# Performance work log

Measured on AMD Instinct MI355X. Metric: run time of the kernel, lower is better.

## Reference

```python
import jax, jax.numpy as jnp
import numpy as np
from jax import lax

B, CIN, H, W = 32, 128, 64, 64
COUT, K, NK, HID = 128, 3, 4, 32
TEMP = 34.0
PAD = 1


def setup_inputs() -> dict:
    key = jax.random.key(0)
    k1, k2, k3, k4 = jax.random.split(key, 4)
    x = jax.random.normal(k1, (B, CIN, H, W), dtype=jnp.float32)
    fc1_w = jax.random.normal(k2, (HID, CIN), dtype=jnp.float32) * (2.0 / CIN) ** 0.5
    fc2_w = jax.random.normal(k3, (NK, HID), dtype=jnp.float32) * (2.0 / HID) ** 0.5
    fc2_b = jnp.zeros((NK,), dtype=jnp.float32)
    weight = jax.random.normal(k4, (NK, COUT, CIN, K, K), dtype=jnp.float32) * 0.05
    bias = jnp.zeros((NK, COUT), dtype=jnp.float32)
    return {"x": x, "fc1_w": fc1_w, "fc2_w": fc2_w, "fc2_b": fc2_b,
            "weight": weight, "bias": bias}


def _per_sample_conv(xi, wi):
    # xi: [CIN, H, W], wi: [COUT, CIN, K, K]
    out = lax.conv_general_dilated(
        xi[None], wi,
        window_strides=(1, 1),
        padding=[(PAD, PAD), (PAD, PAD)],
        dimension_numbers=("NCHW", "OIHW", "NCHW"))
    return out[0]  # [COUT, H', W']


def reference(x, fc1_w, fc2_w, fc2_b, weight, bias):
    # attention: global avg pool -> 1x1 conv (matmul) -> relu -> 1x1 conv -> softmax
    context = jnp.mean(x, axis=(2, 3))                      # [B, CIN]
    hid = jax.nn.relu(context @ fc1_w.T)                    # [B, HID]
    logits = hid @ fc2_w.T + fc2_b                          # [B, NK]
    att = jax.nn.softmax(logits / TEMP, axis=1)             # [B, NK]
    # aggregate per-sample kernels and biases
    agg_w = jnp.einsum("bk,koihw->boihw", att, weight)      # [B, COUT, CIN, K, K]
    agg_b = att @ bias                                      # [B, COUT]
    # per-sample convolution (equivalent to the groups=B trick in torch)
    out = jax.vmap(_per_sample_conv)(x, agg_w)              # [B, COUT, H, W]
    return out + agg_b[:, :, None, None]
```

## Files before the change

### kernel.cpp

```cpp
#include <hip/hip_runtime.h>

#define B_    32
#define CIN_  128
#define H_    64
#define W_    64
#define COUT_ 128
#define NK_   4
#define HID_  32
#define TEMP_ 34.0f

typedef short bf16x8 __attribute__((ext_vector_type(8)));
typedef float f32x16 __attribute__((ext_vector_type(16)));

__device__ __forceinline__ short f2bf(float f) {
    union { float f; unsigned u; } c; c.f = f;
    unsigned r = (c.u + 0x7FFFu + ((c.u >> 16) & 1u)) >> 16;
    return (short)r;
}

__global__ __launch_bounds__(64) void k_context(const float* __restrict__ x,
                                                float* __restrict__ ctx) {
    const int bc = blockIdx.x;
    const float* p = x + (size_t)bc * (H_ * W_);
    const int lane = threadIdx.x;
    float s = 0.f;
    for (int i = lane * 4; i < H_ * W_; i += 64 * 4) {
        float4 v = *(const float4*)(p + i);
        s += v.x + v.y + v.z + v.w;
    }
    for (int off = 32; off > 0; off >>= 1) s += __shfl_down(s, off, 64);
    if (lane == 0) ctx[bc] = s * (1.0f / (H_ * W_));
}

__global__ __launch_bounds__(256) void k_aggw(const float* __restrict__ ctx,
        const float* __restrict__ fc1w, const float* __restrict__ fc2w,
        const float* __restrict__ fc2b, const float* __restrict__ bias,
        const float* __restrict__ weight, short* __restrict__ aggwt,
        float* __restrict__ aggb) {
    __shared__ float hidp[8][32];
    __shared__ float shid[32];
    __shared__ float satt[NK_];
    __shared__ float sbuf[2304];
    const int t = threadIdx.x;
    const int blk = blockIdx.x;
    const int b = blk >> 6;
    const int co0 = (blk & 63) * 2;
    {
        const int hh = t & 31, part = t >> 5;
        const float* c  = ctx + b * CIN_ + part * 16;
        const float* f1 = fc1w + hh * CIN_ + part * 16;
        float s = 0.f;
#pragma unroll
        for (int j = 0; j < 16; ++j) s += c[j] * f1[j];
        hidp[part][hh] = s;
    }
    __syncthreads();
    if (t < 32) {
        float s = 0.f;
#pragma unroll
        for (int p = 0; p < 8; ++p) s += hidp[p][t];
        shid[t] = fmaxf(s, 0.f);
    }
    __syncthreads();
    if (t == 0) {
        float lg[NK_]; float mx = -1e30f;
#pragma unroll
        for (int k = 0; k < NK_; ++k) {
            float s = fc2b[k];
            for (int hh = 0; hh < HID_; ++hh) s += shid[hh] * fc2w[k * HID_ + hh];
            lg[k] = s / TEMP_; mx = fmaxf(mx, lg[k]);
        }
        float den = 0.f;
#pragma unroll
        for (int k = 0; k < NK_; ++k) { lg[k] = expf(lg[k] - mx); den += lg[k]; }
        const float rd = 1.0f / den;
#pragma unroll
        for (int k = 0; k < NK_; ++k) satt[k] = lg[k] * rd;
    }
    __syncthreads();
    const float a0 = satt[0], a1 = satt[1], a2 = satt[2], a3 = satt[3];

    if ((t & 127) == 0) {
        const int co = co0 + (t >> 7);
        aggb[b * COUT_ + co] = a0 * bias[co] + a1 * bias[COUT_ + co]
                             + a2 * bias[2 * COUT_ + co] + a3 * bias[3 * COUT_ + co];
    }

    const size_t kstride = (size_t)COUT_ * CIN_ * 9;
    const float* W0 = weight + (size_t)co0 * (CIN_ * 9);
#pragma unroll
    for (int jj = 0; jj < 3; ++jj) {
        const int i4 = jj * 256 + t;
        if (i4 < 576) {
            const float4 w0 = *(const float4*)(W0 + i4 * 4);
            const float4 w1 = *(const float4*)(W0 + kstride + i4 * 4);
            const float4 w2 = *(const float4*)(W0 + 2 * kstride + i4 * 4);
            const float4 w3 = *(const float4*)(W0 + 3 * kstride + i4 * 4);
            float4 r;
            r.x = a0 * w0.x + a1 * w1.x + a2 * w2.x + a3 * w3.x;
            r.y = a0 * w0.y + a1 * w1.y + a2 * w2.y + a3 * w3.y;
            r.z = a0 * w0.z + a1 * w1.z + a2 * w2.z + a3 * w3.z;
            r.w = a0 * w0.w + a1 * w1.w + a2 * w2.w + a3 * w3.w;
            *(float4*)(&sbuf[i4 * 4]) = r;
        }
    }
    __syncthreads();
#pragma unroll
    for (int jj = 0; jj < 2; ++jj) {
        const int g = jj * 256 + t;
        if (g < 288) {
            const int coL = (g >= 144) ? 1 : 0;
            const int gg = g - coL * 144;
            const int r  = gg >> 4;
            const int oc = gg & 15;
            const int co = co0 + coL;
            bf16x8 v;
#pragma unroll
            for (int e = 0; e < 8; ++e)
                v[e] = f2bf(sbuf[(coL * 128 + oc * 8 + e) * 9 + r]);
            short* dst = aggwt
                + ((size_t)(((b * 4 + (co >> 5)) * 9 + r) * 8 + (oc >> 1)) * 512)
                + ((co & 31) * 2 + (oc & 1)) * 8;
            *(bf16x8*)dst = v;
        }
    }
}

#define RBY 8448
#define RSH 4224
__global__ __launch_bounds__(256, 2) void k_conv(const float* __restrict__ x,
        const short* __restrict__ aggwt, const float* __restrict__ aggb,
        float* __restrict__ out) {
    __shared__ short xt[6 * RSH];
    const int tid = threadIdx.x;
    const int blk = blockIdx.x;
    const int b = blk & 31;
    const int h0 = (blk >> 5) * 4;
    const int lane = tid & 63;
    const int wv = tid >> 6;
    const int l31 = lane & 31;
    const int lane5 = lane >> 5;

    if (tid < 96) {
        const int row = tid >> 4;
        const int q = tid & 15;
        const int cl = (q < 8) ? q : (512 + q);
        *(int4*)(&xt[row * RSH + cl * 8]) = make_int4(0, 0, 0, 0);
    }

    f32x16 acc[8];
#pragma unroll
    for (int t = 0; t < 8; ++t)
#pragma unroll
        for (int k = 0; k < 16; ++k) acc[t][k] = 0.f;

    const short* Ap = aggwt + (size_t)(b * 4 + wv) * (9 * 8 * 512)
                            + (size_t)(l31 * 2 + lane5) * 8;

#pragma unroll
    for (int k = 0; k < 12; ++k) {
        const int task = k * 4 + wv;
        const int row = task >> 3;
        const int g = task & 7;
        const int in_h = h0 - 1 + row;
        bf16x8 v = (bf16x8){0, 0, 0, 0, 0, 0, 0, 0};
        if (in_h >= 0 && in_h < H_) {
            const float* gp = x + (((size_t)b * CIN_ + g * 8) * H_ + in_h) * W_ + lane;
            float f[8];
#pragma unroll
            for (int j = 0; j < 8; ++j) f[j] = gp[j * (H_ * W_)];
#pragma unroll
            for (int j = 0; j < 8; ++j) v[j] = f2bf(f[j]);
        }
        *(bf16x8*)(&xt[row * RSH + ((lane + 1) * 8 + ((g + lane) & 7)) * 8]) = v;
    }
    __syncthreads();

#pragma unroll
    for (int kc = 0; kc < 8; ++kc) {
        float sf[3][8];
        if (kc < 4) {
#pragma unroll
            for (int k = 0; k < 3; ++k) {
                const int task = k * 4 + wv;
                const int row = task >> 1;
                const int j = task & 1;
                const int in_h = h0 - 1 + row;
                if (in_h >= 0 && in_h < H_) {
                    const float* gp = x + (((size_t)b * CIN_ + 64 + (2 * kc + j) * 8) * H_
                                           + in_h) * W_ + lane;
#pragma unroll
                    for (int jj = 0; jj < 8; ++jj) sf[k][jj] = gp[jj * (H_ * W_)];
                }
            }
        }
        bf16x8 av[9];
#pragma unroll
        for (int r = 0; r < 9; ++r)
            av[r] = *(const bf16x8*)(Ap + ((size_t)(r * 8 + kc)) * 512);
        const int kcl = kc & 3;
        __builtin_amdgcn_s_setprio(1);
#pragma unroll
        for (int ir = 0; ir < 6; ++ir) {
            bf16x8 bv[2][3];
#pragma unroll
            for (int i = 0; i < 2; ++i)
#pragma unroll
                for (int kw = 0; kw < 3; ++kw) {
                    const int s = i * 32 + l31 + kw;
                    const int off = 16 * ((2 * kcl + lane5 + s - 1) & 7);
                    bv[i][kw] = *(const bf16x8*)((const char*)xt + ir * RBY + s * 128 + off);
                }
#pragma unroll
            for (int orr = 0; orr < 4; ++orr) {
                if (orr <= ir && ir <= orr + 2) {
                    const int kh = ir - orr;
#pragma unroll
                    for (int i = 0; i < 2; ++i)
#pragma unroll
                        for (int kw = 0; kw < 3; ++kw)
                            acc[orr * 2 + i] = __builtin_amdgcn_mfma_f32_32x32x16_bf16(
                                av[kh * 3 + kw], bv[i][kw], acc[orr * 2 + i], 0, 0, 0);
                }
            }
        }
        __builtin_amdgcn_s_setprio(0);
        if (kc <= 4) __syncthreads();
        if (kc < 4) {
#pragma unroll
            for (int k = 0; k < 3; ++k) {
                const int task = k * 4 + wv;
                const int row = task >> 1;
                const int j = task & 1;
                const int in_h = h0 - 1 + row;
                const int g = 2 * kc + j;
                bf16x8 v = (bf16x8){0, 0, 0, 0, 0, 0, 0, 0};
                if (in_h >= 0 && in_h < H_) {
#pragma unroll
                    for (int jj = 0; jj < 8; ++jj) v[jj] = f2bf(sf[k][jj]);
                }
                *(bf16x8*)(&xt[row * RSH + ((lane + 1) * 8 + ((g + lane) & 7)) * 8]) = v;
            }
        }
    }

    const float* ab = aggb + b * COUT_;
#pragma unroll
    for (int orr = 0; orr < 4; ++orr) {
#pragma unroll
        for (int i = 0; i < 2; ++i) {
            const int hh = h0 + orr;
            const int w = i * 32 + l31;
            float* op = out + ((size_t)b * COUT_ * H_ + hh) * W_ + w;
            const f32x16 a = acc[orr * 2 + i];
#pragma unroll
            for (int reg = 0; reg < 16; ++reg) {
                const int co = wv * 32 + (reg & 3) + 8 * (reg >> 2) + 4 * lane5;
                op[(size_t)co * (H_ * W_)] = a[reg] + ab[co];
            }
        }
    }
}

extern "C" void kernel_launch(void* const* d_in, const int* in_sizes, int n_in,
                              void* d_out, int out_size, void* d_ws, size_t ws_size,
                              hipStream_t stream) {
    const float* x    = (const float*)d_in[0];
    const float* fc1w = (const float*)d_in[1];
    const float* fc2w = (const float*)d_in[2];
    const float* fc2b = (const float*)d_in[3];
    const float* wgt  = (const float*)d_in[4];
    const float* bias = (const float*)d_in[5];
    float* out = (float*)d_out;

    char* ws = (char*)d_ws;
    float* ctx   = (float*)(ws + 0);
    float* aggb  = (float*)(ws + 16384);
    short* aggwt = (short*)(ws + 65536);

    k_context<<<dim3(B_ * CIN_), dim3(64), 0, stream>>>(x, ctx);
    k_aggw<<<dim3(B_ * (COUT_ / 2)), dim3(256), 0, stream>>>(
        ctx, fc1w, fc2w, fc2b, bias, wgt, aggwt, aggb);
    k_conv<<<dim3(B_ * (H_ / 4)), dim3(256), 0, stream>>>(x, aggwt, aggb, out);
}
```

Before: 165.4 us.

## Fuse context, weight aggregation and conv into one cooperative kernel with grid syncs

Replaces the three separate launches (pooling, attention/weight aggregation, conv) with one cooperative kernel of 512 blocks. Two grid-wide barriers separate the phases, and each phase's work is remapped onto the 512 blocks. The shared-memory tile is unioned with the aggregation scratch. The goal is to remove launch gaps and tail effects between the small pre-conv kernels. In exchange it depends on all 512 blocks being co-resident (2 per CU), pays the cost of the grid syncs, and falls back to the old path if the cooperative launch fails.

```diff
diff --git a/kernel.cpp b/kernel.cpp
--- a/kernel.cpp
+++ b/kernel.cpp
@@ -1,4 +1,6 @@
 #include <hip/hip_runtime.h>
+#include <hip/hip_cooperative_groups.h>
+namespace cg = cooperative_groups;
 
 #define B_    32
 #define CIN_  128
@@ -16,6 +18,255 @@
     union { float f; unsigned u; } c; c.f = f;
     unsigned r = (c.u + 0x7FFFu + ((c.u >> 16) & 1u)) >> 16;
     return (short)r;
+}
+
+#define RBY 8448
+#define RSH 4224
+
+__global__ __launch_bounds__(256, 2) void k_fused(
+        const float* __restrict__ x, const float* __restrict__ fc1w,
+        const float* __restrict__ fc2w, const float* __restrict__ fc2b,
+        const float* __restrict__ weight, const float* __restrict__ bias,
+        float* __restrict__ out, float* __restrict__ ctx,
+        short* __restrict__ aggwt, float* __restrict__ aggb) {
+    __shared__ union {
+        short xt[6 * RSH];
+        struct {
+            float hidp[8][32];
+            float shid[32];
+            float satt[NK_];
+            float sbuf[9216];
+        } p2;
+    } sm;
+    const int tid = threadIdx.x;
+    const int blk = blockIdx.x;
+
+    {
+        const int row = blk * 8 + (tid >> 5);
+        const int l32 = tid & 31;
+        const float* p = x + (size_t)row * (H_ * W_);
+        float s = 0.f;
+#pragma unroll
+        for (int k = 0; k < 32; ++k) {
+            float4 v = *(const float4*)(p + l32 * 4 + k * 128);
+            s += v.x + v.y + v.z + v.w;
+        }
+#pragma unroll
+        for (int off = 16; off > 0; off >>= 1) s += __shfl_down(s, off, 32);
+        if (l32 == 0) ctx[row] = s * (1.0f / (H_ * W_));
+    }
+    cg::this_grid().sync();
+
+    {
+        const int b2 = blk >> 4;
+        const int co0 = (blk & 15) * 8;
+        {
+            const int hh = tid & 31, part = tid >> 5;
+            const float* c  = ctx + b2 * CIN_ + part * 16;
+            const float* f1 = fc1w + hh * CIN_ + part * 16;
+            float s = 0.f;
+#pragma unroll
+            for (int j = 0; j < 16; ++j) s += c[j] * f1[j];
+            sm.p2.hidp[part][hh] = s;
+        }
+        __syncthreads();
+        if (tid < 32) {
+            float s = 0.f;
+#pragma unroll
+            for (int p = 0; p < 8; ++p) s += sm.p2.hidp[p][tid];
+            sm.p2.shid[tid] = fmaxf(s, 0.f);
+        }
+        __syncthreads();
+        if (tid == 0) {
+            float lg[NK_]; float mx = -1e30f;
+#pragma unroll
+            for (int k = 0; k < NK_; ++k) {
+                float s = fc2b[k];
+                for (int hh = 0; hh < HID_; ++hh) s += sm.p2.shid[hh] * fc2w[k * HID_ + hh];
+                lg[k] = s / TEMP_; mx = fmaxf(mx, lg[k]);
+            }
+            float den = 0.f;
+#pragma unroll
+            for (int k = 0; k < NK_; ++k) { lg[k] = expf(lg[k] - mx); den += lg[k]; }
+            const float rd = 1.0f / den;
+#pragma unroll
+            for (int k = 0; k < NK_; ++k) sm.p2.satt[k] = lg[k] * rd;
+        }
+        __syncthreads();
+        const float a0 = sm.p2.satt[0], a1 = sm.p2.satt[1],
+                    a2 = sm.p2.satt[2], a3 = sm.p2.satt[3];
+
+        if (tid < 8) {
+            const int co = co0 + tid;
+            aggb[b2 * COUT_ + co] = a0 * bias[co] + a1 * bias[COUT_ + co]
+                                  + a2 * bias[2 * COUT_ + co] + a3 * bias[3 * COUT_ + co];
+        }
+
+        const size_t kstride = (size_t)COUT_ * CIN_ * 9;
+        const float* W0 = weight + (size_t)co0 * (CIN_ * 9);
+#pragma unroll
+        for (int jj = 0; jj < 9; ++jj) {
+            const int i4 = jj * 256 + tid;
+            const float4 w0 = *(const float4*)(W0 + i4 * 4);
+            const float4 w1 = *(const float4*)(W0 + kstride + i4 * 4);
+            const float4 w2 = *(const float4*)(W0 + 2 * kstride + i4 * 4);
+            const float4 w3 = *(const float4*)(W0 + 3 * kstride + i4 * 4);
+            float4 r;
+            r.x = a0 * w0.x + a1 * w1.x + a2 * w2.x + a3 * w3.x;
+            r.y = a0 * w0.y + a1 * w1.y + a2 * w2.y + a3 * w3.y;
+            r.z = a0 * w0.z + a1 * w1.z + a2 * w2.z + a3 * w3.z;
+            r.w = a0 * w0.w + a1 * w1.w + a2 * w2.w + a3 * w3.w;
+            *(float4*)(&sm.p2.sbuf[i4 * 4]) = r;
+        }
+        __syncthreads();
+#pragma unroll
+        for (int jj = 0; jj < 5; ++jj) {
+            const int g = jj * 256 + tid;
+            if (g < 1152) {
+                const int coL = g / 144;
+                const int gg = g - coL * 144;
+                const int r  = gg >> 4;
+                const int oc = gg & 15;
+                const int co = co0 + coL;
+                bf16x8 v;
+#pragma unroll
+                for (int e = 0; e < 8; ++e)
+                    v[e] = f2bf(sm.p2.sbuf[(coL * 128 + oc * 8 + e) * 9 + r]);
+                short* dst = aggwt
+                    + ((size_t)(((b2 * 4 + (co >> 5)) * 9 + r) * 8 + (oc >> 1)) * 512)
+                    + ((co & 31) * 2 + (oc & 1)) * 8;
+                *(bf16x8*)dst = v;
+            }
+        }
+    }
+    cg::this_grid().sync();
+
+    const int b = blk & 31;
+    const int h0 = (blk >> 5) * 4;
+    const int lane = tid & 63;
+    const int wv = tid >> 6;
+    const int l31 = lane & 31;
+    const int lane5 = lane >> 5;
+
+    if (tid < 96) {
+        const int row = tid >> 4;
+        const int q = tid & 15;
+        const int cl = (q < 8) ? q : (512 + q);
+        *(int4*)(&sm.xt[row * RSH + cl * 8]) = make_int4(0, 0, 0, 0);
+    }
+
+    f32x16 acc[8];
+#pragma unroll
+    for (int t = 0; t < 8; ++t)
+#pragma unroll
+        for (int k = 0; k < 16; ++k) acc[t][k] = 0.f;
+
+    const short* Ap = aggwt + (size_t)(b * 4 + wv) * (9 * 8 * 512)
+                            + (size_t)(l31 * 2 + lane5) * 8;
+
+#pragma unroll
+    for (int k = 0; k < 12; ++k) {
+        const int task = k * 4 + wv;
+        const int row = task >> 3;
+        const int g = task & 7;
+        const int in_h = h0 - 1 + row;
+        bf16x8 v = (bf16x8){0, 0, 0, 0, 0, 0, 0, 0};
+        if (in_h >= 0 && in_h < H_) {
+            const float* gp = x + (((size_t)b * CIN_ + g * 8) * H_ + in_h) * W_ + lane;
+            float f[8];
+#pragma unroll
+            for (int j = 0; j < 8; ++j) f[j] = gp[j * (H_ * W_)];
+#pragma unroll
+            for (int j = 0; j < 8; ++j) v[j] = f2bf(f[j]);
+        }
+        *(bf16x8*)(&sm.xt[row * RSH + ((lane + 1) * 8 + ((g + lane) & 7)) * 8]) = v;
+    }
+    __syncthreads();
+
+#pragma unroll
+    for (int kc = 0; kc < 8; ++kc) {
+        float sf[3][8];
+        if (kc < 4) {
+#pragma unroll
+            for (int k = 0; k < 3; ++k) {
+                const int task = k * 4 + wv;
+                const int row = task >> 1;
+                const int j = task & 1;
+                const int in_h = h0 - 1 + row;
+                if (in_h >= 0 && in_h < H_) {
+                    const float* gp = x + (((size_t)b * CIN_ + 64 + (2 * kc + j) * 8) * H_
+                                           + in_h) * W_ + lane;
+#pragma unroll
+                    for (int jj = 0; jj < 8; ++jj) sf[k][jj] = gp[jj * (H_ * W_)];
+                }
+            }
+        }
+        bf16x8 av[9];
+#pragma unroll
+        for (int r = 0; r < 9; ++r)
+            av[r] = *(const bf16x8*)(Ap + ((size_t)(r * 8 + kc)) * 512);
+        const int kcl = kc & 3;
+        __builtin_amdgcn_s_setprio(1);
+#pragma unroll
+        for (int ir = 0; ir < 6; ++ir) {
+            bf16x8 bv[2][3];
+#pragma unroll
+            for (int i = 0; i < 2; ++i)
+#pragma unroll
+                for (int kw = 0; kw < 3; ++kw) {
+                    const int s = i * 32 + l31 + kw;
+                    const int off = 16 * ((2 * kcl + lane5 + s - 1) & 7);
+                    bv[i][kw] = *(const bf16x8*)((const char*)sm.xt + ir * RBY + s * 128 + off);
+                }
+#pragma unroll
+            for (int orr = 0; orr < 4; ++orr) {
+                if (orr <= ir && ir <= orr + 2) {
+                    const int kh = ir - orr;
+#pragma unroll
+                    for (int i = 0; i < 2; ++i)
+#pragma unroll
+                        for (int kw = 0; kw < 3; ++kw)
+                            acc[orr * 2 + i] = __builtin_amdgcn_mfma_f32_32x32x16_bf16(
+                                av[kh * 3 + kw], bv[i][kw], acc[orr * 2 + i], 0, 0, 0);
+                }
+            }
+        }
+        __builtin_amdgcn_s_setprio(0);
+        if (kc <= 4) __syncthreads();
+        if (kc < 4) {
+#pragma unroll
+            for (int k = 0; k < 3; ++k) {
+                const int task = k * 4 + wv;
+                const int row = task >> 1;
+                const int j = task & 1;
+                const int in_h = h0 - 1 + row;
+                const int g = 2 * kc + j;
+                bf16x8 v = (bf16x8){0, 0, 0, 0, 0, 0, 0, 0};
+                if (in_h >= 0 && in_h < H_) {
+#pragma unroll
+                    for (int jj = 0; jj < 8; ++jj) v[jj] = f2bf(sf[k][jj]);
+                }
+                *(bf16x8*)(&sm.xt[row * RSH + ((lane + 1) * 8 + ((g + lane) & 7)) * 8]) = v;
+            }
+        }
+    }
+
+    const float* ab = aggb + b * COUT_;
+#pragma unroll
+    for (int orr = 0; orr < 4; ++orr) {
+#pragma unroll
+        for (int i = 0; i < 2; ++i) {
+            const int hh = h0 + orr;
+            const int w = i * 32 + l31;
+            float* op = out + ((size_t)b * COUT_ * H_ + hh) * W_ + w;
+            const f32x16 a = acc[orr * 2 + i];
+#pragma unroll
+            for (int reg = 0; reg < 16; ++reg) {
+                const int co = wv * 32 + (reg & 3) + 8 * (reg >> 2) + 4 * lane5;
+                op[(size_t)co * (H_ * W_)] = a[reg] + ab[co];
+            }
+        }
+    }
 }
 
 __global__ __launch_bounds__(64) void k_context(const float* __restrict__ x,
@@ -79,13 +330,11 @@
     }
     __syncthreads();
     const float a0 = satt[0], a1 = satt[1], a2 = satt[2], a3 = satt[3];
-
     if ((t & 127) == 0) {
         const int co = co0 + (t >> 7);
         aggb[b * COUT_ + co] = a0 * bias[co] + a1 * bias[COUT_ + co]
                              + a2 * bias[2 * COUT_ + co] + a3 * bias[3 * COUT_ + co];
     }
-
     const size_t kstride = (size_t)COUT_ * CIN_ * 9;
     const float* W0 = weight + (size_t)co0 * (CIN_ * 9);
 #pragma unroll
@@ -126,8 +375,6 @@
     }
 }
 
-#define RBY 8448
-#define RSH 4224
 __global__ __launch_bounds__(256, 2) void k_conv(const float* __restrict__ x,
         const short* __restrict__ aggwt, const float* __restrict__ aggb,
         float* __restrict__ out) {
@@ -140,23 +387,19 @@
     const int wv = tid >> 6;
     const int l31 = lane & 31;
     const int lane5 = lane >> 5;
-
     if (tid < 96) {
         const int row = tid >> 4;
         const int q = tid & 15;
         const int cl = (q < 8) ? q : (512 + q);
         *(int4*)(&xt[row * RSH + cl * 8]) = make_int4(0, 0, 0, 0);
     }
-
     f32x16 acc[8];
 #pragma unroll
     for (int t = 0; t < 8; ++t)
 #pragma unroll
         for (int k = 0; k < 16; ++k) acc[t][k] = 0.f;
-
     const short* Ap = aggwt + (size_t)(b * 4 + wv) * (9 * 8 * 512)
                             + (size_t)(l31 * 2 + lane5) * 8;
-
 #pragma unroll
     for (int k = 0; k < 12; ++k) {
         const int task = k * 4 + wv;
@@ -175,7 +418,6 @@
         *(bf16x8*)(&xt[row * RSH + ((lane + 1) * 8 + ((g + lane) & 7)) * 8]) = v;
     }
     __syncthreads();
-
 #pragma unroll
     for (int kc = 0; kc < 8; ++kc) {
         float sf[3][8];
@@ -243,7 +485,6 @@
             }
         }
     }
-
     const float* ab = aggb + b * COUT_;
 #pragma unroll
     for (int orr = 0; orr < 4; ++orr) {
@@ -278,8 +519,15 @@
     float* aggb  = (float*)(ws + 16384);
     short* aggwt = (short*)(ws + 65536);
 
-    k_context<<<dim3(B_ * CIN_), dim3(64), 0, stream>>>(x, ctx);
-    k_aggw<<<dim3(B_ * (COUT_ / 2)), dim3(256), 0, stream>>>(
-        ctx, fc1w, fc2w, fc2b, bias, wgt, aggwt, aggb);
-    k_conv<<<dim3(B_ * (H_ / 4)), dim3(256), 0, stream>>>(x, aggwt, aggb, out);
+    void* kargs[] = {(void*)&x, (void*)&fc1w, (void*)&fc2w, (void*)&fc2b,
+                     (void*)&wgt, (void*)&bias, (void*)&out,
+                     (void*)&ctx, (void*)&aggwt, (void*)&aggb};
+    hipError_t e = hipLaunchCooperativeKernel((const void*)k_fused,
+                                              dim3(512), dim3(256), kargs, 0, stream);
+    if (e != hipSuccess) {
+        k_context<<<dim3(B_ * CIN_), dim3(64), 0, stream>>>(x, ctx);
+        k_aggw<<<dim3(B_ * (COUT_ / 2)), dim3(256), 0, stream>>>(
+            ctx, fc1w, fc2w, fc2b, bias, wgt, aggwt, aggb);
+        k_conv<<<dim3(B_ * (H_ / 4)), dim3(256), 0, stream>>>(x, aggwt, aggb, out);
+    }
 }
```

After: 299.2 us. 1.81x slower.
